# Optimization experiments

Measured on AMD Instinct MI355X. Metric: run time of the kernel, lower is better.

The kernel has to match this reference:

```python
import jax, jax.numpy as jnp
import numpy as np
from jax import lax

DIM = 8        # per-head dim
HEADS = 32     # inp // dim
EPS = 1e-15    # linear-attention eps
BN_EPS = 1e-5  # torch BatchNorm2d default eps


def _conv(x, w, groups=1, pad=0):
    return lax.conv_general_dilated(
        x, w, window_strides=(1, 1), padding=[(pad, pad), (pad, pad)],
        feature_group_count=groups,
        dimension_numbers=('NCHW', 'OIHW', 'NCHW'))


def setup_inputs() -> dict:
    key = jax.random.key(0)
    ks = jax.random.split(key, 9)
    B, C, H, W = 8, 256, 64, 64
    td = HEADS * DIM  # 256
    x = jax.random.normal(ks[0], (B, C, H, W), jnp.float32)
    w_qkv = jax.random.normal(ks[1], (3 * td, C, 1, 1), jnp.float32) * 0.05
    w_dw = jax.random.normal(ks[2], (3 * td, 1, 5, 5), jnp.float32) * 0.05
    w_pw = jax.random.normal(ks[3], (3 * td, (3 * td) // (3 * HEADS), 1, 1), jnp.float32) * 0.05
    w_proj = jax.random.normal(ks[4], (C, 2 * td, 1, 1), jnp.float32) * 0.05
    bn_gamma = 1.0 + 0.1 * jax.random.normal(ks[5], (C,), jnp.float32)
    bn_beta = 0.1 * jax.random.normal(ks[6], (C,), jnp.float32)
    bn_mean = 0.1 * jax.random.normal(ks[7], (C,), jnp.float32)
    bn_var = jnp.ones((C,), jnp.float32)
    return dict(x=x, w_qkv=w_qkv, w_dw=w_dw, w_pw=w_pw, w_proj=w_proj,
                bn_gamma=bn_gamma, bn_beta=bn_beta, bn_mean=bn_mean, bn_var=bn_var)


def reference(x, w_qkv, w_dw, w_pw, w_proj, bn_gamma, bn_beta, bn_mean, bn_var):
    B, _, H, W = x.shape
    # qkv: 1x1 conv, no bias/norm/act
    qkv = _conv(x, w_qkv)                                   # (B, 3*td, H, W)
    # aggreg branch: depthwise 5x5 then grouped 1x1 (groups = 3*heads)
    agg = _conv(qkv, w_dw, groups=w_dw.shape[0], pad=2)
    agg = _conv(agg, w_pw, groups=3 * HEADS)
    ms = jnp.concatenate([qkv, agg], axis=1)                # (B, 2*3*td, H, W)
    # relu linear attention
    G = ms.shape[1] // (3 * DIM)                            # 2*heads = 64
    t = ms.reshape(B, G, 3 * DIM, H * W).transpose(0, 1, 3, 2)  # (B, G, N, 3d)
    q = jax.nn.relu(t[..., :DIM])
    k = jax.nn.relu(t[..., DIM:2 * DIM])
    v = t[..., 2 * DIM:]
    v = jnp.pad(v, ((0, 0), (0, 0), (0, 0), (0, 1)), constant_values=1.0)  # ones trick
    kv = jnp.einsum('bgnd,bgne->bgde', k, v)                # (B, G, d, d+1)
    out = jnp.einsum('bgnd,bgde->bgne', q, kv)              # (B, G, N, d+1)
    out = out[..., :-1] / (out[..., -1:] + EPS)
    out = out.transpose(0, 1, 3, 2).reshape(B, G * DIM, H, W)  # (B, 2*td, H, W)
    # proj: 1x1 conv + BatchNorm2d (eval mode), no act
    out = _conv(out, w_proj)
    inv = jax.lax.rsqrt(bn_var + BN_EPS)
    out = (out - bn_mean[:, None, None]) * (inv * bn_gamma)[:, None, None] + bn_beta[:, None, None]
    return out
```

## Files before the change

### kernel.cpp

```cpp
#include <hip/hip_runtime.h>

typedef __bf16 bf16;
typedef __bf16 bf16x4 __attribute__((ext_vector_type(4)));
typedef __bf16 bf16x8 __attribute__((ext_vector_type(8)));
typedef float f32x4 __attribute__((ext_vector_type(4)));

#define NPIX 4096

__global__ __launch_bounds__(256) void split_x(
    const float* __restrict__ x,
    bf16* __restrict__ xTh, bf16* __restrict__ xTm, bf16* __restrict__ xTl)
{
    const int pix = blockIdx.x * 256 + threadIdx.x;
    const int k0  = blockIdx.y * 32;
    const int b   = blockIdx.z;

    const float* __restrict__ src = x + ((size_t)b * 256 + k0) * NPIX + pix;
    float v[32];
#pragma unroll
    for (int kk = 0; kk < 32; ++kk) v[kk] = src[(size_t)kk * NPIX];

    const size_t drow = ((size_t)b * NPIX + pix) * 256 + k0;
#pragma unroll
    for (int c = 0; c < 4; ++c) {
        bf16x8 vh, vm, vl;
#pragma unroll
        for (int j = 0; j < 8; ++j) {
            float val = v[c * 8 + j];
            bf16 h = (bf16)val; float r  = val - (float)h;
            bf16 m = (bf16)r;   float r2 = r - (float)m;
            vh[j] = h; vm[j] = m; vl[j] = (bf16)r2;
        }
        *(bf16x8*)(xTh + drow + c * 8) = vh;
        *(bf16x8*)(xTm + drow + c * 8) = vm;
        *(bf16x8*)(xTl + drow + c * 8) = vl;
    }
}

__global__ __launch_bounds__(256, 2) void qkv_mfma(
    const float* __restrict__ A,
    const bf16* __restrict__ xTh,
    const bf16* __restrict__ xTm,
    const bf16* __restrict__ xTl,
    float* __restrict__ C)
{
    __shared__ bf16 As[3][128][40];

    const int tid  = threadIdx.x;
    const int lane = tid & 63;
    const int wv   = tid >> 6;
    const int col  = lane & 15;
    const int quad = lane >> 4;
    const int wm   = (wv >> 1) * 64;
    const int wn   = (wv & 1) * 64;
    const int n0   = blockIdx.x * 128;
    const int m0   = blockIdx.y * 128;
    const int b    = blockIdx.z;

    const int arow = tid >> 1;
    const int akc  = (tid & 1) * 16;

    const size_t xoff = ((size_t)b * NPIX + n0 + wn) * 256;

    f32x4 acc[4][4] = {};

    float av[16];
    {
        const float* ap = A + (size_t)(m0 + arow) * 256 + akc;
        *(float4*)&av[0]  = *(const float4*)(ap);
        *(float4*)&av[4]  = *(const float4*)(ap + 4);
        *(float4*)&av[8]  = *(const float4*)(ap + 8);
        *(float4*)&av[12] = *(const float4*)(ap + 12);
    }

    for (int k0 = 0; k0 < 256; k0 += 32) {
        __syncthreads();

#pragma unroll
        for (int c = 0; c < 4; ++c) {
            bf16x4 vh, vm, vl;
#pragma unroll
            for (int j = 0; j < 4; ++j) {
                float val = av[c * 4 + j];
                bf16 h = (bf16)val; float r  = val - (float)h;
                bf16 m = (bf16)r;   float r2 = r - (float)m;
                vh[j] = h; vm[j] = m; vl[j] = (bf16)r2;
            }
            *(bf16x4*)&As[0][arow][akc + c * 4] = vh;
            *(bf16x4*)&As[1][arow][akc + c * 4] = vm;
            *(bf16x4*)&As[2][arow][akc + c * 4] = vl;
        }

        if (k0 + 32 < 256) {
            const float* ap = A + (size_t)(m0 + arow) * 256 + k0 + 32 + akc;
            *(float4*)&av[0]  = *(const float4*)(ap);
            *(float4*)&av[4]  = *(const float4*)(ap + 4);
            *(float4*)&av[8]  = *(const float4*)(ap + 8);
            *(float4*)&av[12] = *(const float4*)(ap + 12);
        }

        __syncthreads();

        bf16x8 bh[4], bm[4], bl[4];
#pragma unroll
        for (int t = 0; t < 4; ++t) {
            const size_t brow = xoff + (size_t)(t * 16 + col) * 256 + k0 + quad * 8;
            bh[t] = *(const bf16x8*)(xTh + brow);
            bm[t] = *(const bf16x8*)(xTm + brow);
            bl[t] = *(const bf16x8*)(xTl + brow);
        }
        bf16x8 af[4][3];
#pragma unroll
        for (int s = 0; s < 4; ++s)
#pragma unroll
            for (int p = 0; p < 3; ++p)
                af[s][p] = *(const bf16x8*)&As[p][wm + s * 16 + col][quad * 8];

#pragma unroll
        for (int t = 0; t < 4; ++t)
#pragma unroll
            for (int s = 0; s < 4; ++s)
                acc[s][t] = __builtin_amdgcn_mfma_f32_16x16x32_bf16(af[s][2], bh[t], acc[s][t], 0, 0, 0);
#pragma unroll
        for (int t = 0; t < 4; ++t)
#pragma unroll
            for (int s = 0; s < 4; ++s)
                acc[s][t] = __builtin_amdgcn_mfma_f32_16x16x32_bf16(af[s][0], bl[t], acc[s][t], 0, 0, 0);
#pragma unroll
        for (int t = 0; t < 4; ++t)
#pragma unroll
            for (int s = 0; s < 4; ++s)
                acc[s][t] = __builtin_amdgcn_mfma_f32_16x16x32_bf16(af[s][1], bm[t], acc[s][t], 0, 0, 0);
#pragma unroll
        for (int t = 0; t < 4; ++t)
#pragma unroll
            for (int s = 0; s < 4; ++s)
                acc[s][t] = __builtin_amdgcn_mfma_f32_16x16x32_bf16(af[s][1], bh[t], acc[s][t], 0, 0, 0);
#pragma unroll
        for (int t = 0; t < 4; ++t)
#pragma unroll
            for (int s = 0; s < 4; ++s)
                acc[s][t] = __builtin_amdgcn_mfma_f32_16x16x32_bf16(af[s][0], bm[t], acc[s][t], 0, 0, 0);
#pragma unroll
        for (int t = 0; t < 4; ++t)
#pragma unroll
            for (int s = 0; s < 4; ++s)
                acc[s][t] = __builtin_amdgcn_mfma_f32_16x16x32_bf16(af[s][0], bh[t], acc[s][t], 0, 0, 0);
    }

    float* __restrict__ Cp = C + (size_t)b * 768 * NPIX;
#pragma unroll
    for (int s = 0; s < 4; ++s)
#pragma unroll
        for (int t = 0; t < 4; ++t)
#pragma unroll
            for (int r = 0; r < 4; ++r) {
                const int m = m0 + wm + s * 16 + quad * 4 + r;
                const int n = n0 + wn + t * 16 + col;
                Cp[(size_t)m * NPIX + n] = acc[s][t][r];
            }
}

__global__ __launch_bounds__(256) void dwpw(
    const float* __restrict__ qkv,
    const float* __restrict__ w_dw,
    const float* __restrict__ w_pw,
    float* __restrict__ agg)
{
    __shared__ float sm[8][20][20];
    __shared__ float wdw[8][25];
    __shared__ float wpw[8][8];

    const int tid = threadIdx.x;
    const int p   = blockIdx.z % 96;
    const int b   = blockIdx.z / 96;
    const int y0  = blockIdx.y * 16;
    const int x0  = blockIdx.x * 16;

    const float* __restrict__ src = qkv + ((size_t)b * 768 + 8 * p) * NPIX;

    for (int i = tid; i < 8 * 400; i += 256) {
        int c = i / 400, r = i % 400;
        int sy = r / 20, sx = r % 20;
        int gy = y0 + sy - 2, gx = x0 + sx - 2;
        float v = 0.0f;
        if ((unsigned)gy < 64u && (unsigned)gx < 64u)
            v = src[(size_t)c * NPIX + gy * 64 + gx];
        sm[c][sy][sx] = v;
    }
    if (tid < 200) {
        int c = tid / 25, t = tid % 25;
        wdw[c][t] = w_dw[(size_t)(8 * p + c) * 25 + t];
    }
    if (tid < 64) {
        int o = tid / 8, i = tid % 8;
        wpw[o][i] = w_pw[(size_t)(8 * p + o) * 8 + i];
    }
    __syncthreads();

    const int ty = tid >> 4, tx = tid & 15;

    float d[8];
#pragma unroll
    for (int c = 0; c < 8; ++c) {
        float s = 0.0f;
#pragma unroll
        for (int ky = 0; ky < 5; ++ky)
#pragma unroll
            for (int kx = 0; kx < 5; ++kx)
                s += wdw[c][ky * 5 + kx] * sm[c][ty + ky][tx + kx];
        d[c] = s;
    }

    float* __restrict__ dst = agg + ((size_t)b * 768 + 8 * p) * NPIX + (y0 + ty) * 64 + (x0 + tx);
#pragma unroll
    for (int o = 0; o < 8; ++o) {
        float s = 0.0f;
#pragma unroll
        for (int i = 0; i < 8; ++i) s += wpw[o][i] * d[i];
        dst[(size_t)o * NPIX] = s;
    }
}

__global__ __launch_bounds__(256) void kv_reduce(
    const float* __restrict__ qkv, const float* __restrict__ agg,
    float* __restrict__ kvb)
{
    const int g = blockIdx.x, b = blockIdx.y;
    const float* __restrict__ src = (g < 32) ? qkv : agg;
    const float* __restrict__ base = src + ((size_t)b * 768 + 24 * (g & 31)) * NPIX;

    float acc[72];
#pragma unroll
    for (int i = 0; i < 72; ++i) acc[i] = 0.0f;

    for (int i4 = threadIdx.x; i4 < NPIX / 4; i4 += 256) {
        float4 kf[8], vf[8];
#pragma unroll
        for (int d = 0; d < 8; ++d) {
            float4 t = ((const float4*)(base + (size_t)(8 + d) * NPIX))[i4];
            kf[d].x = fmaxf(0.0f, t.x); kf[d].y = fmaxf(0.0f, t.y);
            kf[d].z = fmaxf(0.0f, t.z); kf[d].w = fmaxf(0.0f, t.w);
        }
#pragma unroll
        for (int e = 0; e < 8; ++e)
            vf[e] = ((const float4*)(base + (size_t)(16 + e) * NPIX))[i4];
#pragma unroll
        for (int d = 0; d < 8; ++d) {
#pragma unroll
            for (int e = 0; e < 8; ++e)
                acc[d * 9 + e] += kf[d].x * vf[e].x + kf[d].y * vf[e].y +
                                  kf[d].z * vf[e].z + kf[d].w * vf[e].w;
            acc[d * 9 + 8] += kf[d].x + kf[d].y + kf[d].z + kf[d].w;
        }
    }

    const int lane = threadIdx.x & 63;
    const int wv   = threadIdx.x >> 6;
#pragma unroll
    for (int i = 0; i < 72; ++i) {
        float v = acc[i];
        v += __shfl_xor(v, 32, 64);
        v += __shfl_xor(v, 16, 64);
        v += __shfl_xor(v, 8, 64);
        v += __shfl_xor(v, 4, 64);
        v += __shfl_xor(v, 2, 64);
        v += __shfl_xor(v, 1, 64);
        acc[i] = v;
    }
    __shared__ float red[4][72];
    if (lane == 0) {
#pragma unroll
        for (int i = 0; i < 72; ++i) red[wv][i] = acc[i];
    }
    __syncthreads();
    if (threadIdx.x < 72)
        kvb[((size_t)b * 64 + g) * 72 + threadIdx.x] =
            red[0][threadIdx.x] + red[1][threadIdx.x] +
            red[2][threadIdx.x] + red[3][threadIdx.x];
}

__global__ __launch_bounds__(256) void attn_fused(
    const float* __restrict__ qkv, const float* __restrict__ agg,
    const float* __restrict__ kvb,
    bf16* __restrict__ attTh, bf16* __restrict__ attTm)
{
    const int b   = blockIdx.y;
    const int n0  = blockIdx.x * 32;
    const int tid = threadIdx.x;
    const int p   = tid & 31;
    const int c   = tid >> 5;

    __shared__ float kvs[64 * 72];
    for (int i = tid; i < 64 * 72; i += 256) kvs[i] = kvb[(size_t)b * 64 * 72 + i];
    __syncthreads();

    const int n = n0 + p;
    const size_t orow = ((size_t)b * NPIX + n) * 512;

#pragma unroll
    for (int gi = 0; gi < 8; ++gi) {
        const int g = c * 8 + gi;
        const float* __restrict__ src = (g < 32) ? qkv : agg;
        const float* __restrict__ base = src + ((size_t)b * 768 + 24 * (g & 31)) * NPIX + n;

        float q[8];
#pragma unroll
        for (int d = 0; d < 8; ++d) q[d] = fmaxf(0.0f, base[(size_t)d * NPIX]);

        const float* kv = &kvs[g * 72];
        float den = 1e-15f;
#pragma unroll
        for (int d = 0; d < 8; ++d) den = fmaf(q[d], kv[d * 9 + 8], den);
        float inv = 1.0f / den;
#pragma unroll
        for (int d = 0; d < 8; ++d) q[d] *= inv;

        bf16x8 vh, vm;
#pragma unroll
        for (int e = 0; e < 8; ++e) {
            float o = 0.0f;
#pragma unroll
            for (int d = 0; d < 8; ++d) o = fmaf(q[d], kv[d * 9 + e], o);
            bf16 h = (bf16)o;
            vh[e] = h;
            vm[e] = (bf16)(o - (float)h);
        }
        *(bf16x8*)(attTh + orow + g * 8) = vh;
        *(bf16x8*)(attTm + orow + g * 8) = vm;
    }
}

__global__ __launch_bounds__(256, 2) void proj_mfma(
    const float* __restrict__ A,
    const bf16* __restrict__ Bh,
    const bf16* __restrict__ Bm,
    float* __restrict__ C,
    const float* __restrict__ bn_g, const float* __restrict__ bn_b,
    const float* __restrict__ bn_m, const float* __restrict__ bn_v)
{
    __shared__ bf16 As[2][128][40];

    const int tid  = threadIdx.x;
    const int lane = tid & 63;
    const int wv   = tid >> 6;
    const int col  = lane & 15;
    const int quad = lane >> 4;
    const int wm   = (wv >> 1) * 64;
    const int wn   = (wv & 1) * 64;
    const int n0   = blockIdx.x * 128;
    const int m0   = blockIdx.y * 128;
    const int b    = blockIdx.z;

    const int arow = tid >> 1;
    const int akc  = (tid & 1) * 16;

    const size_t boff = ((size_t)b * NPIX + n0 + wn) * 512;

    f32x4 acc[4][4] = {};

    float av[16];
    {
        const float* ap = A + (size_t)(m0 + arow) * 512 + akc;
        *(float4*)&av[0]  = *(const float4*)(ap);
        *(float4*)&av[4]  = *(const float4*)(ap + 4);
        *(float4*)&av[8]  = *(const float4*)(ap + 8);
        *(float4*)&av[12] = *(const float4*)(ap + 12);
    }

    for (int k0 = 0; k0 < 512; k0 += 32) {
        __syncthreads();

#pragma unroll
        for (int c = 0; c < 4; ++c) {
            bf16x4 vh, vm;
#pragma unroll
            for (int j = 0; j < 4; ++j) {
                float val = av[c * 4 + j];
                bf16 h = (bf16)val;
                vh[j] = h; vm[j] = (bf16)(val - (float)h);
            }
            *(bf16x4*)&As[0][arow][akc + c * 4] = vh;
            *(bf16x4*)&As[1][arow][akc + c * 4] = vm;
        }

        if (k0 + 32 < 512) {
            const float* ap = A + (size_t)(m0 + arow) * 512 + k0 + 32 + akc;
            *(float4*)&av[0]  = *(const float4*)(ap);
            *(float4*)&av[4]  = *(const float4*)(ap + 4);
            *(float4*)&av[8]  = *(const float4*)(ap + 8);
            *(float4*)&av[12] = *(const float4*)(ap + 12);
        }

        __syncthreads();

        bf16x8 bh[4], bm2[4];
#pragma unroll
        for (int t = 0; t < 4; ++t) {
            const size_t brow = boff + (size_t)(t * 16 + col) * 512 + k0 + quad * 8;
            bh[t]  = *(const bf16x8*)(Bh + brow);
            bm2[t] = *(const bf16x8*)(Bm + brow);
        }
        bf16x8 af[4][2];
#pragma unroll
        for (int s = 0; s < 4; ++s) {
            af[s][0] = *(const bf16x8*)&As[0][wm + s * 16 + col][quad * 8];
            af[s][1] = *(const bf16x8*)&As[1][wm + s * 16 + col][quad * 8];
        }

#pragma unroll
        for (int t = 0; t < 4; ++t)
#pragma unroll
            for (int s = 0; s < 4; ++s)
                acc[s][t] = __builtin_amdgcn_mfma_f32_16x16x32_bf16(af[s][1], bh[t], acc[s][t], 0, 0, 0);
#pragma unroll
        for (int t = 0; t < 4; ++t)
#pragma unroll
            for (int s = 0; s < 4; ++s)
                acc[s][t] = __builtin_amdgcn_mfma_f32_16x16x32_bf16(af[s][0], bm2[t], acc[s][t], 0, 0, 0);
#pragma unroll
        for (int t = 0; t < 4; ++t)
#pragma unroll
            for (int s = 0; s < 4; ++s)
                acc[s][t] = __builtin_amdgcn_mfma_f32_16x16x32_bf16(af[s][0], bh[t], acc[s][t], 0, 0, 0);
    }

    float* __restrict__ Cp = C + (size_t)b * 256 * NPIX;
#pragma unroll
    for (int s = 0; s < 4; ++s) {
#pragma unroll
        for (int r = 0; r < 4; ++r) {
            const int m = m0 + wm + s * 16 + quad * 4 + r;
            const float sc  = (1.0f / sqrtf(bn_v[m] + 1e-5f)) * bn_g[m];
            const float off = bn_b[m] - bn_m[m] * sc;
#pragma unroll
            for (int t = 0; t < 4; ++t) {
                const int n = n0 + wn + t * 16 + col;
                Cp[(size_t)m * NPIX + n] = acc[s][t][r] * sc + off;
            }
        }
    }
}

extern "C" void kernel_launch(void* const* d_in, const int* in_sizes, int n_in,
                              void* d_out, int out_size, void* d_ws, size_t ws_size,
                              hipStream_t stream) {
    const float* x      = (const float*)d_in[0];
    const float* w_qkv  = (const float*)d_in[1];
    const float* w_dw   = (const float*)d_in[2];
    const float* w_pw   = (const float*)d_in[3];
    const float* w_proj = (const float*)d_in[4];
    const float* bn_g   = (const float*)d_in[5];
    const float* bn_b   = (const float*)d_in[6];
    const float* bn_m   = (const float*)d_in[7];
    const float* bn_v   = (const float*)d_in[8];
    float* out = (float*)d_out;

    char* ws = (char*)d_ws;
    float* qkv  = (float*)ws;
    float* agg  = (float*)(ws + 100663296ull);
    char*  r3   = ws + 201326592ull;
    bf16*  xTh  = (bf16*)r3;
    bf16*  xTm  = (bf16*)(r3 + 16777216ull);
    bf16*  xTl  = (bf16*)(r3 + 33554432ull);
    bf16*  attTh = (bf16*)r3;
    bf16*  attTm = (bf16*)(r3 + 33554432ull);
    float* kvb  = (float*)d_out;

    split_x<<<dim3(16, 8, 8), dim3(256), 0, stream>>>(x, xTh, xTm, xTl);

    qkv_mfma<<<dim3(32, 6, 8), dim3(256), 0, stream>>>(w_qkv, xTh, xTm, xTl, qkv);

    dwpw<<<dim3(4, 4, 8 * 96), dim3(256), 0, stream>>>(qkv, w_dw, w_pw, agg);

    kv_reduce<<<dim3(64, 8), dim3(256), 0, stream>>>(qkv, agg, kvb);

    attn_fused<<<dim3(128, 8), dim3(256), 0, stream>>>(qkv, agg, kvb, attTh, attTm);

    proj_mfma<<<dim3(32, 2, 8), dim3(256), 0, stream>>>(
        w_proj, attTh, attTm, out, bn_g, bn_b, bn_m, bn_v);
}
```

Baseline: 472.2 us.

## Retile depthwise+pointwise conv to full-width rows with float4 register blocking

The dwpw kernel now tiles 16 full-width image rows per block instead of 16x16 tiles. It loads the halo with float4 global reads and computes 4 adjacent output pixels per thread from register-cached shared rows. Weights are read straight from global memory (uniform, scalar-cacheable) rather than staged in shared memory, and outputs are written as float4. The goal is to cut the redundant halo loads, the shared-memory traffic and the index arithmetic. In exchange the block count drops to a quarter and each thread holds more registers.

```diff
diff --git a/kernel.cpp b/kernel.cpp
--- a/kernel.cpp
+++ b/kernel.cpp
@@ -167,58 +167,75 @@
     const float* __restrict__ w_pw,
     float* __restrict__ agg)
 {
-    __shared__ float sm[8][20][20];
-    __shared__ float wdw[8][25];
-    __shared__ float wpw[8][8];
+    __shared__ float sm[8][20][72];
 
     const int tid = threadIdx.x;
-    const int p   = blockIdx.z % 96;
-    const int b   = blockIdx.z / 96;
-    const int y0  = blockIdx.y * 16;
-    const int x0  = blockIdx.x * 16;
+    const int y0  = blockIdx.x * 16;
+    const int p   = blockIdx.y;
+    const int b   = blockIdx.z;
 
     const float* __restrict__ src = qkv + ((size_t)b * 768 + 8 * p) * NPIX;
 
-    for (int i = tid; i < 8 * 400; i += 256) {
-        int c = i / 400, r = i % 400;
-        int sy = r / 20, sx = r % 20;
-        int gy = y0 + sy - 2, gx = x0 + sx - 2;
-        float v = 0.0f;
-        if ((unsigned)gy < 64u && (unsigned)gx < 64u)
-            v = src[(size_t)c * NPIX + gy * 64 + gx];
-        sm[c][sy][sx] = v;
-    }
-    if (tid < 200) {
-        int c = tid / 25, t = tid % 25;
-        wdw[c][t] = w_dw[(size_t)(8 * p + c) * 25 + t];
-    }
-    if (tid < 64) {
-        int o = tid / 8, i = tid % 8;
-        wpw[o][i] = w_pw[(size_t)(8 * p + o) * 8 + i];
+#pragma unroll
+    for (int it = 0; it < 10; ++it) {
+        int idx = tid + it * 256;
+        int c  = idx / 320;
+        int r  = idx % 320;
+        int sy = r >> 4;
+        int x4 = (r & 15) * 4;
+        int gy = y0 + sy - 2;
+        float4 v = {0.f, 0.f, 0.f, 0.f};
+        if ((unsigned)gy < 64u)
+            v = *(const float4*)(src + (size_t)c * NPIX + gy * 64 + x4);
+        *(float4*)&sm[c][sy][4 + x4] = v;
+    }
+    if (tid < 160) {
+        int c = tid / 20, sy = tid % 20;
+        sm[c][sy][2] = 0.f; sm[c][sy][3] = 0.f;
+        sm[c][sy][68] = 0.f; sm[c][sy][69] = 0.f;
     }
     __syncthreads();
 
-    const int ty = tid >> 4, tx = tid & 15;
-
-    float d[8];
+    const int ty = tid >> 4;
+    const int x0 = (tid & 15) * 4;
+
+    float d[8][4];
 #pragma unroll
     for (int c = 0; c < 8; ++c) {
-        float s = 0.0f;
-#pragma unroll
-        for (int ky = 0; ky < 5; ++ky)
-#pragma unroll
-            for (int kx = 0; kx < 5; ++kx)
-                s += wdw[c][ky * 5 + kx] * sm[c][ty + ky][tx + kx];
-        d[c] = s;
-    }
-
-    float* __restrict__ dst = agg + ((size_t)b * 768 + 8 * p) * NPIX + (y0 + ty) * 64 + (x0 + tx);
+        float a0 = 0.f, a1 = 0.f, a2 = 0.f, a3 = 0.f;
+        const float* __restrict__ wc = w_dw + (size_t)(8 * p + c) * 25;
+#pragma unroll
+        for (int ky = 0; ky < 5; ++ky) {
+            float r[12];
+            *(float4*)&r[0] = *(const float4*)&sm[c][ty + ky][x0];
+            *(float4*)&r[4] = *(const float4*)&sm[c][ty + ky][x0 + 4];
+            *(float4*)&r[8] = *(const float4*)&sm[c][ty + ky][x0 + 8];
+#pragma unroll
+            for (int kx = 0; kx < 5; ++kx) {
+                const float wv = wc[ky * 5 + kx];
+                a0 = fmaf(wv, r[2 + 0 + kx], a0);
+                a1 = fmaf(wv, r[2 + 1 + kx], a1);
+                a2 = fmaf(wv, r[2 + 2 + kx], a2);
+                a3 = fmaf(wv, r[2 + 3 + kx], a3);
+            }
+        }
+        d[c][0] = a0; d[c][1] = a1; d[c][2] = a2; d[c][3] = a3;
+    }
+
+    float* __restrict__ dst = agg + ((size_t)b * 768 + 8 * p) * NPIX + (y0 + ty) * 64 + x0;
 #pragma unroll
     for (int o = 0; o < 8; ++o) {
-        float s = 0.0f;
-#pragma unroll
-        for (int i = 0; i < 8; ++i) s += wpw[o][i] * d[i];
-        dst[(size_t)o * NPIX] = s;
+        const float* __restrict__ wo = w_pw + (size_t)(8 * p + o) * 8;
+        float4 s = {0.f, 0.f, 0.f, 0.f};
+#pragma unroll
+        for (int i = 0; i < 8; ++i) {
+            const float wv = wo[i];
+            s.x = fmaf(wv, d[i][0], s.x);
+            s.y = fmaf(wv, d[i][1], s.y);
+            s.z = fmaf(wv, d[i][2], s.z);
+            s.w = fmaf(wv, d[i][3], s.w);
+        }
+        *(float4*)(dst + (size_t)o * NPIX) = s;
     }
 }
 
@@ -471,7 +488,7 @@
 
     qkv_mfma<<<dim3(32, 6, 8), dim3(256), 0, stream>>>(w_qkv, xTh, xTm, xTl, qkv);
 
-    dwpw<<<dim3(4, 4, 8 * 96), dim3(256), 0, stream>>>(qkv, w_dw, w_pw, agg);
+    dwpw<<<dim3(4, 96, 8), dim3(256), 0, stream>>>(qkv, w_dw, w_pw, agg);
 
     kv_reduce<<<dim3(64, 8), dim3(256), 0, stream>>>(qkv, agg, kvb);
 
```

Result: faster. 430.3 us (-8.9%).
